# Optimization experiments

Measured on AMD Instinct MI355X. Metric: run time of the kernel, lower is better.

The kernel has to match this reference:

```python
import jax, jax.numpy as jnp
import numpy as np

NUM_NODES = 100000
EMBED_DIM = 128
COMP_DIM = 64
T = 8
NSUB = 50000


def layer_norm(x, g, b, eps=1e-5):
    mu = jnp.mean(x, axis=-1, keepdims=True)
    var = jnp.mean((x - mu) ** 2, axis=-1, keepdims=True)
    return (x - mu) * jax.lax.rsqrt(var + eps) * g + b


def setup_inputs() -> dict:
    key = jax.random.key(0)
    ks = jax.random.split(key, 12)
    D, C = EMBED_DIM, COMP_DIM
    s = lambda n: 1.0 / np.sqrt(n)
    return {
        "x": jax.random.normal(ks[0], (T * NSUB, D), dtype=jnp.float32),
        "indices": jax.random.randint(ks[1], (T, NSUB), 0, NUM_NODES, dtype=jnp.int64),
        "bd": jax.random.normal(ks[2], (NUM_NODES, D), dtype=jnp.float32),
        "ln_d_g": jnp.ones((D,), jnp.float32), "ln_d_b": jnp.zeros((D,), jnp.float32),
        "Wd1": jax.random.normal(ks[3], (D, 2 * D), jnp.float32) * s(D),
        "bd1": jnp.zeros((2 * D,), jnp.float32),
        "Wd2": jax.random.normal(ks[4], (2 * D, C), jnp.float32) * s(2 * D),
        "bd2": jnp.zeros((C,), jnp.float32),
        "ln_u_g": jnp.ones((C,), jnp.float32), "ln_u_b": jnp.zeros((C,), jnp.float32),
        "Wu1": jax.random.normal(ks[5], (C, 2 * C), jnp.float32) * s(C),
        "bu1": jnp.zeros((2 * C,), jnp.float32),
        "Wu2": jax.random.normal(ks[6], (2 * C, D), jnp.float32) * s(2 * C),
        "bu2": jnp.zeros((D,), jnp.float32),
    }


def reference(x, indices, bd, ln_d_g, ln_d_b, Wd1, bd1, Wd2, bd2,
              ln_u_g, ln_u_b, Wu1, bu1, Wu2, bu2):
    # _to_entire: per-timestep scatter-add of subnode feats into full node table
    x3 = x.reshape(T, NSUB, EMBED_DIM)  # [T, Nsub, D]
    scattered = jax.vmap(
        lambda xt, it: jax.ops.segment_sum(xt, it, num_segments=NUM_NODES)
    )(x3, indices)  # [T, num_nodes, D]
    inp = scattered + bd[None]  # ta + bd (use_bd=True)
    h = layer_norm(inp, ln_d_g, ln_d_b)
    # mlp_d: Linear -> GELU -> Dropout(eval=identity) -> Linear
    h = jax.nn.gelu(h @ Wd1 + bd1, approximate=False) @ Wd2 + bd2  # [T, num_nodes, C]
    # _from_entire: gather activated rows per timestep, then LN + mlp_u
    gathered = jax.vmap(lambda ht, it: ht[it])(h, indices)  # [T, Nsub, C]
    g = gathered.reshape(T * NSUB, COMP_DIM)
    u = layer_norm(g, ln_u_g, ln_u_b)
    out = jax.nn.gelu(u @ Wu1 + bu1, approximate=False) @ Wu2 + bu2  # [T*Nsub, D]
    return out
```

## Files before the change

### kernel.cpp

```cpp
#include <hip/hip_runtime.h>
#include <math.h>

#define NN 100000
#define DD 128
#define CC 64
#define TT 8
#define NS 50000
#define G8 8
#define MAXS2 196
#define TOTW (G8 * MAXS2)

typedef __attribute__((ext_vector_type(4))) float f32x4;
typedef __attribute__((ext_vector_type(8))) short bf16x8;
typedef unsigned short ushort_t;

__device__ __forceinline__ short f2bf(float f) {
    union { float f; unsigned u; } v; v.f = f;
    unsigned r = v.u + 0x7fffu + ((v.u >> 16) & 1u);
    return (short)(r >> 16);
}
__device__ __forceinline__ unsigned pk_bf16(float lo, float hi) {
    unsigned r;
    asm("v_cvt_pk_bf16_f32 %0, %1, %2" : "=v"(r) : "v"(lo), "v"(hi));
    return r;
}
__device__ __forceinline__ float gelu(float x) {
    float t = x + 0.044715f * x * x * x;
    return x / (1.0f + __expf(-1.5957691216f * t));
}

__global__ void prep_all(const float* __restrict__ Wd1, const float* __restrict__ Wd2,
                         const float* __restrict__ Wu1, const float* __restrict__ Wu2,
                         short* __restrict__ pW1, short* __restrict__ pW2,
                         short* __restrict__ pW3, short* __restrict__ pW4) {
    int b = blockIdx.x;
    const float* W; short* dst; int KSTEPS, total, N, s0;
    if (b < 16)      { W = Wd1; dst = pW1; KSTEPS = 4; total = 4096; N = 256; s0 = b * 256; }
    else if (b < 24) { W = Wd2; dst = pW2; KSTEPS = 8; total = 2048; N = 64;  s0 = (b - 16) * 256; }
    else if (b < 28) { W = Wu1; dst = pW3; KSTEPS = 2; total = 1024; N = 128; s0 = (b - 24) * 256; }
    else             { W = Wu2; dst = pW4; KSTEPS = 4; total = 2048; N = 128; s0 = (b - 28) * 256; }
    int s = s0 + threadIdx.x;
    if (s >= total) return;
    int lane = s & 63;
    int ks = (s >> 6) % KSTEPS;
    int n = s / (64 * KSTEPS);
    int kb = ks * 32 + (lane >> 4) * 8;
    int col = n * 16 + (lane & 15);
    bf16x8 o;
    #pragma unroll
    for (int j = 0; j < 8; ++j) o[j] = f2bf(W[(size_t)(kb + j) * N + col]);
    *(bf16x8*)(dst + (size_t)s * 8) = o;
}

__global__ void flagfill_kernel(const int* __restrict__ idx, int* __restrict__ pernode,
                                ushort_t* __restrict__ bucket) {
    int i = blockIdx.x * 256 + threadIdx.x;
    if (i >= G8 * NS) return;
    int g = i / NS, s = i - g * NS;
    int node = idx[i];
    int p = atomicAdd(&pernode[node * 8 + g], 1);
    if (p < 16) bucket[((size_t)node * 8 + g) * 16 + p] = (ushort_t)s;
}

__global__ void compact_kernel(const int* __restrict__ pernode,
                               int* __restrict__ lists, int* __restrict__ cnts) {
    int g = blockIdx.y;
    int node = blockIdx.x * 256 + threadIdx.x;
    bool active = (node < NN) && (pernode[node * 8 + g] > 0);
    unsigned long long m = __ballot(active);
    int lane = threadIdx.x & 63;
    int rank = __popcll(m & ((1ull << lane) - 1ull));
    int nact = __popcll(m);
    int lbase = 0;
    if (lane == 0 && nact > 0) lbase = atomicAdd(&cnts[g], nact);
    lbase = __shfl(lbase, 0);
    if (active) lists[(size_t)g * NS + lbase + rank] = node;
}

__global__ __launch_bounds__(1024, 4) void fused_kernel(
    const float* __restrict__ x, const float* __restrict__ bd,
    const float* __restrict__ lndg, const float* __restrict__ lndb,
    const short* __restrict__ pW1, const short* __restrict__ pW2,
    const short* __restrict__ pW3, const short* __restrict__ pW4,
    const float* __restrict__ bd1, const float* __restrict__ bd2,
    const float* __restrict__ lnug, const float* __restrict__ lnub,
    const float* __restrict__ bu1, const float* __restrict__ bu2,
    const int* __restrict__ lists, const int* __restrict__ cnts,
    const int* __restrict__ pernode, const ushort_t* __restrict__ bucket,
    float* __restrict__ out) {
    __shared__ short sW1[4096 * 8];
    __shared__ short sW2[2048 * 8];
    __shared__ short sW4[2048 * 8];
    __shared__ short sBuf[16][1024];

    const int tid = threadIdx.x;
    for (int s = tid; s < 4096; s += 1024)
        *(bf16x8*)(sW1 + s * 8) = *(const bf16x8*)(pW1 + (size_t)s * 8);
    for (int s = tid; s < 2048; s += 1024)
        *(bf16x8*)(sW2 + s * 8) = *(const bf16x8*)(pW2 + (size_t)s * 8);
    for (int s = tid; s < 2048; s += 1024)
        *(bf16x8*)(sW4 + s * 8) = *(const bf16x8*)(pW4 + (size_t)s * 8);
    __syncthreads();

    const int wave = tid >> 6, lane = tid & 63;
    short* myb = sBuf[wave];
    const int arow = lane & 15;
    const int kgrp = lane >> 4;

    int w = blockIdx.x;
    int node_c = 0, c_c = 0;
    int4 p8_c = {0, 0, 0, 0};
    {
        int g0 = w & 7, strip0 = w >> 3;
        int gi0 = strip0 * 256 + wave * 16 + arow;
        int li0 = gi0 < NS ? gi0 : NS - 1;
        node_c = lists[(size_t)g0 * NS + li0];
        c_c = pernode[node_c * 8 + g0];
        p8_c = *(const int4*)(bucket + ((size_t)node_c * 8 + g0) * 16);
    }

    for (; w < TOTW; w += gridDim.x) {
        const int g = w & 7, strip = w >> 3;
        const int nrows = cnts[g];
        const int row0 = strip * 256 + wave * 16;
        const float* x_g = x + (size_t)g * NS * DD;
        float* out_g = out + (size_t)g * NS * DD;

        const int wn = w + gridDim.x;
        const bool hn = wn < TOTW;
        const int gn = hn ? (wn & 7) : 0;
        const int stripn = hn ? (wn >> 3) : 0;
        int gin = stripn * 256 + wave * 16 + arow;
        int lin = gin < NS ? gin : NS - 1;
        const int node_n = lists[(size_t)gn * NS + lin];
        int c_n;
        int4 p8_n;

        if (strip * 256 < nrows) {
            const int c = c_c;
            const int pr0 = p8_c.x & 0xffff, pr1 = ((unsigned)p8_c.x) >> 16;
            const int pr2 = p8_c.y & 0xffff, pr3 = ((unsigned)p8_c.y) >> 16;
            float v[32];
            {
                const float* bp = bd + (size_t)node_c * DD + kgrp * 8;
                const float* xq0 = x_g + (size_t)pr0 * DD + kgrp * 8;
                const float* xq1 = x_g + (size_t)((c > 1) ? pr1 : pr0) * DD + kgrp * 8;
                const float m1 = (c > 1) ? 1.f : 0.f;
                #pragma unroll
                for (int ks = 0; ks < 4; ++ks) {
                    float4 b0 = *(const float4*)(bp + ks * 32);
                    float4 b1 = *(const float4*)(bp + ks * 32 + 4);
                    float4 a0 = *(const float4*)(xq0 + ks * 32);
                    float4 a1 = *(const float4*)(xq0 + ks * 32 + 4);
                    float4 d0 = *(const float4*)(xq1 + ks * 32);
                    float4 d1 = *(const float4*)(xq1 + ks * 32 + 4);
                    v[ks*8+0] = fmaf(m1, d0.x, b0.x + a0.x);
                    v[ks*8+1] = fmaf(m1, d0.y, b0.y + a0.y);
                    v[ks*8+2] = fmaf(m1, d0.z, b0.z + a0.z);
                    v[ks*8+3] = fmaf(m1, d0.w, b0.w + a0.w);
                    v[ks*8+4] = fmaf(m1, d1.x, b1.x + a1.x);
                    v[ks*8+5] = fmaf(m1, d1.y, b1.y + a1.y);
                    v[ks*8+6] = fmaf(m1, d1.z, b1.z + a1.z);
                    v[ks*8+7] = fmaf(m1, d1.w, b1.w + a1.w);
                }
            }
            if (__any(c > 2)) {
                const float* xq2 = x_g + (size_t)((c > 2) ? pr2 : pr0) * DD + kgrp * 8;
                const float* xq3 = x_g + (size_t)((c > 3) ? pr3 : pr0) * DD + kgrp * 8;
                const float m2 = (c > 2) ? 1.f : 0.f;
                const float m3 = (c > 3) ? 1.f : 0.f;
                #pragma unroll
                for (int ks = 0; ks < 4; ++ks) {
                    float4 a0 = *(const float4*)(xq2 + ks * 32);
                    float4 a1 = *(const float4*)(xq2 + ks * 32 + 4);
                    float4 d0 = *(const float4*)(xq3 + ks * 32);
                    float4 d1 = *(const float4*)(xq3 + ks * 32 + 4);
                    v[ks*8+0] = fmaf(m3, d0.x, fmaf(m2, a0.x, v[ks*8+0]));
                    v[ks*8+1] = fmaf(m3, d0.y, fmaf(m2, a0.y, v[ks*8+1]));
                    v[ks*8+2] = fmaf(m3, d0.z, fmaf(m2, a0.z, v[ks*8+2]));
                    v[ks*8+3] = fmaf(m3, d0.w, fmaf(m2, a0.w, v[ks*8+3]));
                    v[ks*8+4] = fmaf(m3, d1.x, fmaf(m2, a1.x, v[ks*8+4]));
                    v[ks*8+5] = fmaf(m3, d1.y, fmaf(m2, a1.y, v[ks*8+5]));
                    v[ks*8+6] = fmaf(m3, d1.z, fmaf(m2, a1.z, v[ks*8+6]));
                    v[ks*8+7] = fmaf(m3, d1.w, fmaf(m2, a1.w, v[ks*8+7]));
                }
            }
            if (__any(c > 4)) {
                const int pr4 = p8_c.z & 0xffff, pr5 = ((unsigned)p8_c.z) >> 16;
                const int pr6 = p8_c.w & 0xffff, pr7 = ((unsigned)p8_c.w) >> 16;
                const float* xq4 = x_g + (size_t)((c > 4) ? pr4 : pr0) * DD + kgrp * 8;
                const float* xq5 = x_g + (size_t)((c > 5) ? pr5 : pr0) * DD + kgrp * 8;
                const float* xq6 = x_g + (size_t)((c > 6) ? pr6 : pr0) * DD + kgrp * 8;
                const float* xq7 = x_g + (size_t)((c > 7) ? pr7 : pr0) * DD + kgrp * 8;
                const float m4 = (c > 4) ? 1.f : 0.f;
                const float m5 = (c > 5) ? 1.f : 0.f;
                const float m6 = (c > 6) ? 1.f : 0.f;
                const float m7 = (c > 7) ? 1.f : 0.f;
                #pragma unroll
                for (int ks = 0; ks < 4; ++ks) {
                    float4 a0 = *(const float4*)(xq4 + ks * 32);
                    float4 a1 = *(const float4*)(xq4 + ks * 32 + 4);
                    float4 d0 = *(const float4*)(xq5 + ks * 32);
                    float4 d1 = *(const float4*)(xq5 + ks * 32 + 4);
                    float4 e0 = *(const float4*)(xq6 + ks * 32);
                    float4 e1 = *(const float4*)(xq6 + ks * 32 + 4);
                    float4 f0 = *(const float4*)(xq7 + ks * 32);
                    float4 f1 = *(const float4*)(xq7 + ks * 32 + 4);
                    #pragma unroll
                    for (int q = 0; q < 4; ++q) {
                        float av = (&a0.x)[q], dv = (&d0.x)[q], ev = (&e0.x)[q], fv = (&f0.x)[q];
                        v[ks*8+q] = fmaf(m7, fv, fmaf(m6, ev, fmaf(m5, dv, fmaf(m4, av, v[ks*8+q]))));
                        float av1 = (&a1.x)[q], dv1 = (&d1.x)[q], ev1 = (&e1.x)[q], fv1 = (&f1.x)[q];
                        v[ks*8+4+q] = fmaf(m7, fv1, fmaf(m6, ev1, fmaf(m5, dv1, fmaf(m4, av1, v[ks*8+4+q]))));
                    }
                }
            }
            if (__any(c > 8)) {
                const ushort_t* bt = bucket + ((size_t)node_c * 8 + g) * 16;
                for (int j = 8; j < 16; ++j) {
                    const int pj = (j < c) ? bt[j] : pr0;
                    const float mj = (j < c) ? 1.f : 0.f;
                    const float* xq = x_g + (size_t)pj * DD + kgrp * 8;
                    #pragma unroll
                    for (int ks = 0; ks < 4; ++ks) {
                        float4 a0 = *(const float4*)(xq + ks * 32);
                        float4 a1 = *(const float4*)(xq + ks * 32 + 4);
                        v[ks*8+0] = fmaf(mj, a0.x, v[ks*8+0]);
                        v[ks*8+1] = fmaf(mj, a0.y, v[ks*8+1]);
                        v[ks*8+2] = fmaf(mj, a0.z, v[ks*8+2]);
                        v[ks*8+3] = fmaf(mj, a0.w, v[ks*8+3]);
                        v[ks*8+4] = fmaf(mj, a1.x, v[ks*8+4]);
                        v[ks*8+5] = fmaf(mj, a1.y, v[ks*8+5]);
                        v[ks*8+6] = fmaf(mj, a1.z, v[ks*8+6]);
                        v[ks*8+7] = fmaf(mj, a1.w, v[ks*8+7]);
                    }
                }
            }
            float s1 = 0.f;
            #pragma unroll
            for (int j = 0; j < 32; ++j) s1 += v[j];
            s1 += __shfl_xor(s1, 16); s1 += __shfl_xor(s1, 32);
            float mu = s1 * 0.0078125f;
            float s2 = 0.f;
            #pragma unroll
            for (int j = 0; j < 32; ++j) { float d = v[j] - mu; s2 += d * d; }
            s2 += __shfl_xor(s2, 16); s2 += __shfl_xor(s2, 32);
            float rs = rsqrtf(s2 * 0.0078125f + 1e-5f);
            union U8 { bf16x8 v8; unsigned u[4]; };
            bf16x8 afr[4];
            {
                const float* gp = lndg + kgrp * 8;
                const float* bbp = lndb + kgrp * 8;
                #pragma unroll
                for (int ks = 0; ks < 4; ++ks) {
                    float4 g0 = *(const float4*)(gp + ks * 32);
                    float4 g1 = *(const float4*)(gp + ks * 32 + 4);
                    float4 c0 = *(const float4*)(bbp + ks * 32);
                    float4 c1 = *(const float4*)(bbp + ks * 32 + 4);
                    U8 t;
                    t.u[0] = pk_bf16((v[ks*8+0]-mu)*rs*g0.x + c0.x, (v[ks*8+1]-mu)*rs*g0.y + c0.y);
                    t.u[1] = pk_bf16((v[ks*8+2]-mu)*rs*g0.z + c0.z, (v[ks*8+3]-mu)*rs*g0.w + c0.w);
                    t.u[2] = pk_bf16((v[ks*8+4]-mu)*rs*g1.x + c1.x, (v[ks*8+5]-mu)*rs*g1.y + c1.y);
                    t.u[3] = pk_bf16((v[ks*8+6]-mu)*rs*g1.z + c1.z, (v[ks*8+7]-mu)*rs*g1.w + c1.w);
                    afr[ks] = t.v8;
                }
            }
            f32x4 acc2[4];
            #pragma unroll
            for (int n = 0; n < 4; ++n) acc2[n] = (f32x4){0.f, 0.f, 0.f, 0.f};
            for (int ks2 = 0; ks2 < 8; ++ks2) {
                f32x4 a1v[2];
                a1v[0] = (f32x4){0.f, 0.f, 0.f, 0.f};
                a1v[1] = (f32x4){0.f, 0.f, 0.f, 0.f};
                #pragma unroll
                for (int ks1 = 0; ks1 < 4; ++ks1) {
                    #pragma unroll
                    for (int p = 0; p < 2; ++p) {
                        bf16x8 bf = *(const bf16x8*)(sW1 + (size_t)((((2*ks2+p) << 2) | ks1) * 64 + lane) * 8);
                        a1v[p] = __builtin_amdgcn_mfma_f32_16x16x32_bf16(afr[ks1], bf, a1v[p], 0, 0, 0);
                    }
                }
                #pragma unroll
                for (int p = 0; p < 2; ++p) {
                    float bias = bd1[(2*ks2+p) * 16 + arow];
                    #pragma unroll
                    for (int rr = 0; rr < 4; ++rr) {
                        float vv = gelu(a1v[p][rr] + bias);
                        int row = kgrp * 4 + rr;
                        int byte = row * 64 + (((p * 16 + arow) * 2) ^ ((row & 3) << 4));
                        myb[byte >> 1] = f2bf(vv);
                    }
                }
                bf16x8 af2 = *(const bf16x8*)(myb + ((arow * 64 + ((kgrp * 16) ^ ((arow & 3) << 4))) >> 1));
                #pragma unroll
                for (int n2 = 0; n2 < 4; ++n2) {
                    bf16x8 bf = *(const bf16x8*)(sW2 + (size_t)(((n2 << 3) | ks2) * 64 + lane) * 8);
                    acc2[n2] = __builtin_amdgcn_mfma_f32_16x16x32_bf16(af2, bf, acc2[n2], 0, 0, 0);
                }
            }
            c_n = pernode[node_n * 8 + gn];
            p8_n = *(const int4*)(bucket + ((size_t)node_n * 8 + gn) * 16);
            float hv[4][4];
            #pragma unroll
            for (int n2 = 0; n2 < 4; ++n2)
                #pragma unroll
                for (int rr = 0; rr < 4; ++rr)
                    hv[n2][rr] = acc2[n2][rr] + bd2[n2 * 16 + arow];
            float mu_u[4], rs_u[4];
            #pragma unroll
            for (int rr = 0; rr < 4; ++rr) {
                float sr = hv[0][rr] + hv[1][rr] + hv[2][rr] + hv[3][rr];
                sr += __shfl_xor(sr, 1); sr += __shfl_xor(sr, 2);
                sr += __shfl_xor(sr, 4); sr += __shfl_xor(sr, 8);
                mu_u[rr] = sr * 0.015625f;
                float sq = 0.f;
                #pragma unroll
                for (int n2 = 0; n2 < 4; ++n2) { float d = hv[n2][rr] - mu_u[rr]; sq += d * d; }
                sq += __shfl_xor(sq, 1); sq += __shfl_xor(sq, 2);
                sq += __shfl_xor(sq, 4); sq += __shfl_xor(sq, 8);
                rs_u[rr] = rsqrtf(sq * 0.015625f + 1e-5f);
            }
            #pragma unroll
            for (int n2 = 0; n2 < 4; ++n2) {
                int cidx = n2 * 16 + arow;
                float gg = lnug[cidx], bb = lnub[cidx];
                #pragma unroll
                for (int rr = 0; rr < 4; ++rr) {
                    float nv = (hv[n2][rr] - mu_u[rr]) * rs_u[rr] * gg + bb;
                    int row = kgrp * 4 + rr;
                    int byte = row * 128 + ((cidx * 2) ^ ((row & 7) << 4));
                    myb[byte >> 1] = f2bf(nv);
                }
            }
            bf16x8 af3[2];
            #pragma unroll
            for (int ks3 = 0; ks3 < 2; ++ks3)
                af3[ks3] = *(const bf16x8*)(myb + ((arow * 128 + ((ks3 * 64 + kgrp * 16) ^ ((arow & 7) << 4))) >> 1));
            f32x4 acc4[8];
            #pragma unroll
            for (int n = 0; n < 8; ++n) acc4[n] = (f32x4){0.f, 0.f, 0.f, 0.f};
            #pragma unroll
            for (int half = 0; half < 2; ++half) {
                f32x4 a3[4];
                #pragma unroll
                for (int n = 0; n < 4; ++n) a3[n] = (f32x4){0.f, 0.f, 0.f, 0.f};
                #pragma unroll
                for (int ks3 = 0; ks3 < 2; ++ks3) {
                    #pragma unroll
                    for (int n3h = 0; n3h < 4; ++n3h) {
                        int n3 = half * 4 + n3h;
                        bf16x8 bf = *(const bf16x8*)(pW3 + (size_t)(((n3 << 1) | ks3) * 64 + lane) * 8);
                        a3[n3h] = __builtin_amdgcn_mfma_f32_16x16x32_bf16(af3[ks3], bf, a3[n3h], 0, 0, 0);
                    }
                }
                #pragma unroll
                for (int n3h = 0; n3h < 4; ++n3h) {
                    float bias = bu1[(half * 4 + n3h) * 16 + arow];
                    #pragma unroll
                    for (int rr = 0; rr < 4; ++rr) {
                        float vv = gelu(a3[n3h][rr] + bias);
                        int row = kgrp * 4 + rr;
                        int byte = row * 128 + (((n3h * 16 + arow) * 2) ^ ((row & 7) << 4));
                        myb[byte >> 1] = f2bf(vv);
                    }
                }
                #pragma unroll
                for (int k4 = 0; k4 < 2; ++k4) {
                    bf16x8 afu = *(const bf16x8*)(myb + ((arow * 128 + ((k4 * 64 + kgrp * 16) ^ ((arow & 7) << 4))) >> 1));
                    #pragma unroll
                    for (int n4 = 0; n4 < 8; ++n4) {
                        bf16x8 bf = *(const bf16x8*)(sW4 + (size_t)(((n4 << 2) | (half * 2 + k4)) * 64 + lane) * 8);
                        acc4[n4] = __builtin_amdgcn_mfma_f32_16x16x32_bf16(afu, bf, acc4[n4], 0, 0, 0);
                    }
                }
            }
            #pragma unroll
            for (int rr = 0; rr < 4; ++rr) {
                const int src = kgrp * 4 + rr;
                const int c2  = __shfl(c_c, src);
                const unsigned w0 = (unsigned)__shfl(p8_c.x, src);
                const unsigned w1 = (unsigned)__shfl(p8_c.y, src);
                const unsigned w2 = (unsigned)__shfl(p8_c.z, src);
                const unsigned w3 = (unsigned)__shfl(p8_c.w, src);
                const int nd  = __shfl(node_c, src);
                const int gi2 = row0 + kgrp * 4 + rr;
                if (gi2 >= nrows) continue;
                float vals[8];
                #pragma unroll
                for (int n4 = 0; n4 < 8; ++n4) vals[n4] = acc4[n4][rr] + bu2[n4 * 16 + arow];
                {
                    float* op = out_g + (size_t)(w0 & 0xffff) * DD + arow;
                    #pragma unroll
                    for (int n4 = 0; n4 < 8; ++n4) op[n4 * 16] = vals[n4];
                }
                if (c2 > 1) {
                    float* op = out_g + (size_t)(w0 >> 16) * DD + arow;
                    #pragma unroll
                    for (int n4 = 0; n4 < 8; ++n4) op[n4 * 16] = vals[n4];
                }
                if (c2 > 2) {
                    float* op = out_g + (size_t)(w1 & 0xffff) * DD + arow;
                    #pragma unroll
                    for (int n4 = 0; n4 < 8; ++n4) op[n4 * 16] = vals[n4];
                }
                if (c2 > 3) {
                    float* op = out_g + (size_t)(w1 >> 16) * DD + arow;
                    #pragma unroll
                    for (int n4 = 0; n4 < 8; ++n4) op[n4 * 16] = vals[n4];
                }
                if (__any(c2 > 4)) {
                    if (c2 > 4) {
                        float* op = out_g + (size_t)(w2 & 0xffff) * DD + arow;
                        #pragma unroll
                        for (int n4 = 0; n4 < 8; ++n4) op[n4 * 16] = vals[n4];
                    }
                    if (c2 > 5) {
                        float* op = out_g + (size_t)(w2 >> 16) * DD + arow;
                        #pragma unroll
                        for (int n4 = 0; n4 < 8; ++n4) op[n4 * 16] = vals[n4];
                    }
                    if (c2 > 6) {
                        float* op = out_g + (size_t)(w3 & 0xffff) * DD + arow;
                        #pragma unroll
                        for (int n4 = 0; n4 < 8; ++n4) op[n4 * 16] = vals[n4];
                    }
                    if (c2 > 7) {
                        float* op = out_g + (size_t)(w3 >> 16) * DD + arow;
                        #pragma unroll
                        for (int n4 = 0; n4 < 8; ++n4) op[n4 * 16] = vals[n4];
                    }
                }
                if (__any(c2 > 8)) {
                    const ushort_t* bt = bucket + ((size_t)nd * 8 + g) * 16;
                    for (int j = 8; j < 16; ++j) {
                        if (j < c2) {
                            float* op = out_g + (size_t)bt[j] * DD + arow;
                            #pragma unroll
                            for (int n4 = 0; n4 < 8; ++n4) op[n4 * 16] = vals[n4];
                        }
                    }
                }
            }
        } else {
            c_n = pernode[node_n * 8 + gn];
            p8_n = *(const int4*)(bucket + ((size_t)node_n * 8 + gn) * 16);
        }
        node_c = node_n; c_c = c_n; p8_c = p8_n;
    }
}

extern "C" void kernel_launch(void* const* d_in, const int* in_sizes, int n_in,
                              void* d_out, int out_size, void* d_ws, size_t ws_size,
                              hipStream_t stream) {
    const float* x       = (const float*)d_in[0];
    const int*   indices = (const int*)d_in[1];
    const float* bd      = (const float*)d_in[2];
    const float* ln_d_g  = (const float*)d_in[3];
    const float* ln_d_b  = (const float*)d_in[4];
    const float* Wd1     = (const float*)d_in[5];
    const float* bd1     = (const float*)d_in[6];
    const float* Wd2     = (const float*)d_in[7];
    const float* bd2     = (const float*)d_in[8];
    const float* ln_u_g  = (const float*)d_in[9];
    const float* ln_u_b  = (const float*)d_in[10];
    const float* Wu1     = (const float*)d_in[11];
    const float* bu1     = (const float*)d_in[12];
    const float* Wu2     = (const float*)d_in[13];
    const float* bu2     = (const float*)d_in[14];
    float* out = (float*)d_out;

    char* ws = (char*)d_ws;
    size_t o = 0;
    auto alloc_b = [&](size_t bytes) { char* p = ws + o; o = (o + bytes + 255) & ~(size_t)255; return p; };
    int*      pernode = (int*)alloc_b((size_t)NN * 8 * 4);
    int*      cnts    = (int*)alloc_b(8 * 4);
    int*      lists   = (int*)alloc_b((size_t)8 * NS * 4);
    size_t zero_bytes = (size_t)((char*)lists - (char*)pernode) + (size_t)8 * NS * 4;
    ushort_t* bucket  = (ushort_t*)alloc_b((size_t)NN * 8 * 16 * 2);
    short*    pW1     = (short*)alloc_b((size_t)4096 * 16);
    short*    pW2     = (short*)alloc_b((size_t)2048 * 16);
    short*    pW3     = (short*)alloc_b((size_t)1024 * 16);
    short*    pW4     = (short*)alloc_b((size_t)2048 * 16);

    hipMemsetAsync(pernode, 0, zero_bytes, stream);

    prep_all<<<36, 256, 0, stream>>>(Wd1, Wd2, Wu1, Wu2, pW1, pW2, pW3, pW4);
    flagfill_kernel<<<(G8 * NS + 255) / 256, 256, 0, stream>>>(indices, pernode, bucket);
    compact_kernel<<<dim3((NN + 255) / 256, G8), 256, 0, stream>>>(pernode, lists, cnts);
    fused_kernel<<<256, 1024, 0, stream>>>(x, bd, ln_d_g, ln_d_b, pW1, pW2, pW3, pW4,
                                           bd1, bd2, ln_u_g, ln_u_b, bu1, bu2,
                                           lists, cnts, pernode, bucket, out);
}
```

Before: 483.0 us.

## Split work into singleton-node and multi-hit-node paths with separate lists

Nodes hit exactly once per timestep are listed by subnode index and handled on a lean path: one x row plus bd, one output store, no bucket lookup and no masked multi-row accumulation. Nodes hit two or more times go to a second list and keep the bucket-based accumulation and multi-store path. The shared LN/MLP code is factored into device helpers, and the software prefetch of the next tile's node metadata is removed. The aim is to cut wasted loads and divergence on the common singleton case. The cost is two tile ranges to schedule, no cross-iteration prefetch, and a fixed cap of 25000 entries per timestep on the multi-hit list.

```diff
diff --git a/kernel.cpp b/kernel.cpp
--- a/kernel.cpp
+++ b/kernel.cpp
@@ -7,8 +7,9 @@
 #define TT 8
 #define NS 50000
 #define G8 8
-#define MAXS2 196
-#define TOTW (G8 * MAXS2)
+#define T1MAX (G8 * 196)
+#define T2MAX (G8 * 98)
+#define L2CAP 25000
 
 typedef __attribute__((ext_vector_type(4))) float f32x4;
 typedef __attribute__((ext_vector_type(8))) short bf16x8;
@@ -62,30 +63,185 @@
     if (p < 16) bucket[((size_t)node * 8 + g) * 16 + p] = (ushort_t)s;
 }
 
-__global__ void compact_kernel(const int* __restrict__ pernode,
-                               int* __restrict__ lists, int* __restrict__ cnts) {
+__global__ void compact2_kernel(const int* __restrict__ idx, const int* __restrict__ pernode,
+                                int* __restrict__ list1, int* __restrict__ cnts1,
+                                int* __restrict__ list2, int* __restrict__ cnts2) {
     int g = blockIdx.y;
-    int node = blockIdx.x * 256 + threadIdx.x;
-    bool active = (node < NN) && (pernode[node * 8 + g] > 0);
-    unsigned long long m = __ballot(active);
+    int i = blockIdx.x * 256 + threadIdx.x;
     int lane = threadIdx.x & 63;
-    int rank = __popcll(m & ((1ull << lane) - 1ull));
-    int nact = __popcll(m);
-    int lbase = 0;
-    if (lane == 0 && nact > 0) lbase = atomicAdd(&cnts[g], nact);
-    lbase = __shfl(lbase, 0);
-    if (active) lists[(size_t)g * NS + lbase + rank] = node;
+    bool a1 = false;
+    if (i < NS) {
+        int nd = idx[(size_t)g * NS + i];
+        a1 = (pernode[nd * 8 + g] == 1);
+    }
+    unsigned long long m1 = __ballot(a1);
+    int r1 = __popcll(m1 & ((1ull << lane) - 1ull));
+    int c1 = __popcll(m1);
+    int b1 = 0;
+    if (lane == 0 && c1 > 0) b1 = atomicAdd(&cnts1[g], c1);
+    b1 = __shfl(b1, 0);
+    if (a1) list1[(size_t)g * NS + b1 + r1] = i;
+    bool a2 = (i < NN) && (pernode[i * 8 + g] >= 2);
+    unsigned long long m2 = __ballot(a2);
+    int r2 = __popcll(m2 & ((1ull << lane) - 1ull));
+    int c2 = __popcll(m2);
+    int b2 = 0;
+    if (lane == 0 && c2 > 0) b2 = atomicAdd(&cnts2[g], c2);
+    b2 = __shfl(b2, 0);
+    if (a2) list2[(size_t)g * L2CAP + b2 + r2] = i;
+}
+
+__device__ __forceinline__ void mlp_core(
+    const bf16x8 (&afr)[4], short* myb, int arow, int kgrp,
+    const short* sW1, const short* sW2, const short* __restrict__ pW3, const short* sW4,
+    const float* __restrict__ bd1, const float* __restrict__ bd2,
+    const float* __restrict__ lnug, const float* __restrict__ lnub,
+    const float* __restrict__ bu1, f32x4 (&acc4)[8]) {
+    f32x4 acc2[4];
+    #pragma unroll
+    for (int n = 0; n < 4; ++n) acc2[n] = (f32x4){0.f, 0.f, 0.f, 0.f};
+    for (int ks2 = 0; ks2 < 8; ++ks2) {
+        f32x4 a1v[2];
+        a1v[0] = (f32x4){0.f, 0.f, 0.f, 0.f};
+        a1v[1] = (f32x4){0.f, 0.f, 0.f, 0.f};
+        #pragma unroll
+        for (int ks1 = 0; ks1 < 4; ++ks1) {
+            #pragma unroll
+            for (int p = 0; p < 2; ++p) {
+                bf16x8 bf = *(const bf16x8*)(sW1 + (size_t)((((2 * ks2 + p) << 2) | ks1) * 64 + (kgrp * 16 + arow)) * 8);
+                a1v[p] = __builtin_amdgcn_mfma_f32_16x16x32_bf16(afr[ks1], bf, a1v[p], 0, 0, 0);
+            }
+        }
+        #pragma unroll
+        for (int p = 0; p < 2; ++p) {
+            float bias = bd1[(2 * ks2 + p) * 16 + arow];
+            #pragma unroll
+            for (int rr = 0; rr < 4; ++rr) {
+                float vv = gelu(a1v[p][rr] + bias);
+                int row = kgrp * 4 + rr;
+                int byte = row * 64 + (((p * 16 + arow) * 2) ^ ((row & 3) << 4));
+                myb[byte >> 1] = f2bf(vv);
+            }
+        }
+        bf16x8 af2 = *(const bf16x8*)(myb + ((arow * 64 + ((kgrp * 16) ^ ((arow & 3) << 4))) >> 1));
+        #pragma unroll
+        for (int n2 = 0; n2 < 4; ++n2) {
+            bf16x8 bf = *(const bf16x8*)(sW2 + (size_t)(((n2 << 3) | ks2) * 64 + (kgrp * 16 + arow)) * 8);
+            acc2[n2] = __builtin_amdgcn_mfma_f32_16x16x32_bf16(af2, bf, acc2[n2], 0, 0, 0);
+        }
+    }
+    float hv[4][4];
+    #pragma unroll
+    for (int n2 = 0; n2 < 4; ++n2)
+        #pragma unroll
+        for (int rr = 0; rr < 4; ++rr)
+            hv[n2][rr] = acc2[n2][rr] + bd2[n2 * 16 + arow];
+    #pragma unroll
+    for (int rr = 0; rr < 4; ++rr) {
+        float sr = hv[0][rr] + hv[1][rr] + hv[2][rr] + hv[3][rr];
+        sr += __shfl_xor(sr, 1); sr += __shfl_xor(sr, 2);
+        sr += __shfl_xor(sr, 4); sr += __shfl_xor(sr, 8);
+        float mu_u = sr * 0.015625f;
+        float sq = 0.f;
+        #pragma unroll
+        for (int n2 = 0; n2 < 4; ++n2) { float d = hv[n2][rr] - mu_u; sq += d * d; }
+        sq += __shfl_xor(sq, 1); sq += __shfl_xor(sq, 2);
+        sq += __shfl_xor(sq, 4); sq += __shfl_xor(sq, 8);
+        float rs_u = rsqrtf(sq * 0.015625f + 1e-5f);
+        #pragma unroll
+        for (int n2 = 0; n2 < 4; ++n2) {
+            int cidx = n2 * 16 + arow;
+            float nv = (hv[n2][rr] - mu_u) * rs_u * lnug[cidx] + lnub[cidx];
+            int row = kgrp * 4 + rr;
+            int byte = row * 128 + ((cidx * 2) ^ ((row & 7) << 4));
+            myb[byte >> 1] = f2bf(nv);
+        }
+    }
+    bf16x8 af3[2];
+    #pragma unroll
+    for (int ks3 = 0; ks3 < 2; ++ks3)
+        af3[ks3] = *(const bf16x8*)(myb + ((arow * 128 + ((ks3 * 64 + kgrp * 16) ^ ((arow & 7) << 4))) >> 1));
+    #pragma unroll
+    for (int n = 0; n < 8; ++n) acc4[n] = (f32x4){0.f, 0.f, 0.f, 0.f};
+    #pragma unroll
+    for (int half = 0; half < 2; ++half) {
+        f32x4 a3[4];
+        #pragma unroll
+        for (int n = 0; n < 4; ++n) a3[n] = (f32x4){0.f, 0.f, 0.f, 0.f};
+        #pragma unroll
+        for (int ks3 = 0; ks3 < 2; ++ks3) {
+            #pragma unroll
+            for (int n3h = 0; n3h < 4; ++n3h) {
+                int n3 = half * 4 + n3h;
+                bf16x8 bf = *(const bf16x8*)(pW3 + (size_t)(((n3 << 1) | ks3) * 64 + (kgrp * 16 + arow)) * 8);
+                a3[n3h] = __builtin_amdgcn_mfma_f32_16x16x32_bf16(af3[ks3], bf, a3[n3h], 0, 0, 0);
+            }
+        }
+        #pragma unroll
+        for (int n3h = 0; n3h < 4; ++n3h) {
+            float bias = bu1[(half * 4 + n3h) * 16 + arow];
+            #pragma unroll
+            for (int rr = 0; rr < 4; ++rr) {
+                float vv = gelu(a3[n3h][rr] + bias);
+                int row = kgrp * 4 + rr;
+                int byte = row * 128 + (((n3h * 16 + arow) * 2) ^ ((row & 7) << 4));
+                myb[byte >> 1] = f2bf(vv);
+            }
+        }
+        #pragma unroll
+        for (int k4 = 0; k4 < 2; ++k4) {
+            bf16x8 afu = *(const bf16x8*)(myb + ((arow * 128 + ((k4 * 64 + kgrp * 16) ^ ((arow & 7) << 4))) >> 1));
+            #pragma unroll
+            for (int n4 = 0; n4 < 8; ++n4) {
+                bf16x8 bf = *(const bf16x8*)(sW4 + (size_t)(((n4 << 2) | (half * 2 + k4)) * 64 + (kgrp * 16 + arow)) * 8);
+                acc4[n4] = __builtin_amdgcn_mfma_f32_16x16x32_bf16(afu, bf, acc4[n4], 0, 0, 0);
+            }
+        }
+    }
+}
+
+__device__ __forceinline__ void ln_d_pack(
+    const float (&v)[32], int kgrp,
+    const float* __restrict__ lndg, const float* __restrict__ lndb, bf16x8 (&afr)[4]) {
+    float s1 = 0.f;
+    #pragma unroll
+    for (int j = 0; j < 32; ++j) s1 += v[j];
+    s1 += __shfl_xor(s1, 16); s1 += __shfl_xor(s1, 32);
+    float mu = s1 * 0.0078125f;
+    float s2 = 0.f;
+    #pragma unroll
+    for (int j = 0; j < 32; ++j) { float d = v[j] - mu; s2 += d * d; }
+    s2 += __shfl_xor(s2, 16); s2 += __shfl_xor(s2, 32);
+    float rs = rsqrtf(s2 * 0.0078125f + 1e-5f);
+    union U8 { bf16x8 v8; unsigned u[4]; };
+    const float* gp = lndg + kgrp * 8;
+    const float* bbp = lndb + kgrp * 8;
+    #pragma unroll
+    for (int ks = 0; ks < 4; ++ks) {
+        float4 g0 = *(const float4*)(gp + ks * 32);
+        float4 g1 = *(const float4*)(gp + ks * 32 + 4);
+        float4 c0 = *(const float4*)(bbp + ks * 32);
+        float4 c1 = *(const float4*)(bbp + ks * 32 + 4);
+        U8 t;
+        t.u[0] = pk_bf16((v[ks*8+0]-mu)*rs*g0.x + c0.x, (v[ks*8+1]-mu)*rs*g0.y + c0.y);
+        t.u[1] = pk_bf16((v[ks*8+2]-mu)*rs*g0.z + c0.z, (v[ks*8+3]-mu)*rs*g0.w + c0.w);
+        t.u[2] = pk_bf16((v[ks*8+4]-mu)*rs*g1.x + c1.x, (v[ks*8+5]-mu)*rs*g1.y + c1.y);
+        t.u[3] = pk_bf16((v[ks*8+6]-mu)*rs*g1.z + c1.z, (v[ks*8+7]-mu)*rs*g1.w + c1.w);
+        afr[ks] = t.v8;
+    }
 }
 
 __global__ __launch_bounds__(1024, 4) void fused_kernel(
-    const float* __restrict__ x, const float* __restrict__ bd,
+    const float* __restrict__ x, const int* __restrict__ idx,
+    const float* __restrict__ bd,
     const float* __restrict__ lndg, const float* __restrict__ lndb,
     const short* __restrict__ pW1, const short* __restrict__ pW2,
     const short* __restrict__ pW3, const short* __restrict__ pW4,
     const float* __restrict__ bd1, const float* __restrict__ bd2,
     const float* __restrict__ lnug, const float* __restrict__ lnub,
     const float* __restrict__ bu1, const float* __restrict__ bu2,
-    const int* __restrict__ lists, const int* __restrict__ cnts,
+    const int* __restrict__ list1, const int* __restrict__ cnts1,
+    const int* __restrict__ list2, const int* __restrict__ cnts2,
     const int* __restrict__ pernode, const ushort_t* __restrict__ bucket,
     float* __restrict__ out) {
     __shared__ short sW1[4096 * 8];
@@ -107,45 +263,66 @@
     const int arow = lane & 15;
     const int kgrp = lane >> 4;
 
-    int w = blockIdx.x;
-    int node_c = 0, c_c = 0;
-    int4 p8_c = {0, 0, 0, 0};
-    {
-        int g0 = w & 7, strip0 = w >> 3;
-        int gi0 = strip0 * 256 + wave * 16 + arow;
-        int li0 = gi0 < NS ? gi0 : NS - 1;
-        node_c = lists[(size_t)g0 * NS + li0];
-        c_c = pernode[node_c * 8 + g0];
-        p8_c = *(const int4*)(bucket + ((size_t)node_c * 8 + g0) * 16);
-    }
-
-    for (; w < TOTW; w += gridDim.x) {
-        const int g = w & 7, strip = w >> 3;
-        const int nrows = cnts[g];
-        const int row0 = strip * 256 + wave * 16;
-        const float* x_g = x + (size_t)g * NS * DD;
-        float* out_g = out + (size_t)g * NS * DD;
-
-        const int wn = w + gridDim.x;
-        const bool hn = wn < TOTW;
-        const int gn = hn ? (wn & 7) : 0;
-        const int stripn = hn ? (wn >> 3) : 0;
-        int gin = stripn * 256 + wave * 16 + arow;
-        int lin = gin < NS ? gin : NS - 1;
-        const int node_n = lists[(size_t)gn * NS + lin];
-        int c_n;
-        int4 p8_n;
-
-        if (strip * 256 < nrows) {
-            const int c = c_c;
-            const int pr0 = p8_c.x & 0xffff, pr1 = ((unsigned)p8_c.x) >> 16;
-            const int pr2 = p8_c.y & 0xffff, pr3 = ((unsigned)p8_c.y) >> 16;
+    for (int w = blockIdx.x; w < T1MAX + T2MAX; w += gridDim.x) {
+        if (w < T1MAX) {
+            const int g = w & 7, strip = w >> 3;
+            const int n1g = cnts1[g];
+            const int row0 = strip * 256 + wave * 16;
+            if (row0 >= n1g) continue;
+            const float* x_g = x + (size_t)g * NS * DD;
+            float* out_g = out + (size_t)g * NS * DD;
+            const int gi = row0 + arow;
+            const int s_val = list1[(size_t)g * NS + (gi < n1g ? gi : n1g - 1)];
+            const int node = idx[(size_t)g * NS + s_val];
             float v[32];
             {
-                const float* bp = bd + (size_t)node_c * DD + kgrp * 8;
+                const float* xp = x_g + (size_t)s_val * DD + kgrp * 8;
+                const float* bp = bd + (size_t)node * DD + kgrp * 8;
+                #pragma unroll
+                for (int ks = 0; ks < 4; ++ks) {
+                    float4 a0 = *(const float4*)(xp + ks * 32);
+                    float4 a1 = *(const float4*)(xp + ks * 32 + 4);
+                    float4 b0 = *(const float4*)(bp + ks * 32);
+                    float4 b1 = *(const float4*)(bp + ks * 32 + 4);
+                    v[ks*8+0] = a0.x + b0.x; v[ks*8+1] = a0.y + b0.y;
+                    v[ks*8+2] = a0.z + b0.z; v[ks*8+3] = a0.w + b0.w;
+                    v[ks*8+4] = a1.x + b1.x; v[ks*8+5] = a1.y + b1.y;
+                    v[ks*8+6] = a1.z + b1.z; v[ks*8+7] = a1.w + b1.w;
+                }
+            }
+            bf16x8 afr[4];
+            ln_d_pack(v, kgrp, lndg, lndb, afr);
+            f32x4 acc4[8];
+            mlp_core(afr, myb, arow, kgrp, sW1, sW2, pW3, sW4,
+                     bd1, bd2, lnug, lnub, bu1, acc4);
+            #pragma unroll
+            for (int rr = 0; rr < 4; ++rr) {
+                const int src = kgrp * 4 + rr;
+                const int s2v = __shfl(s_val, src);
+                if (row0 + src >= n1g) continue;
+                float* op = out_g + (size_t)s2v * DD + arow;
+                #pragma unroll
+                for (int n4 = 0; n4 < 8; ++n4)
+                    op[n4 * 16] = acc4[n4][rr] + bu2[n4 * 16 + arow];
+            }
+        } else {
+            const int w2 = w - T1MAX;
+            const int g = w2 & 7, strip = w2 >> 3;
+            const int n2g = cnts2[g];
+            const int row0 = strip * 256 + wave * 16;
+            if (row0 >= n2g) continue;
+            const float* x_g = x + (size_t)g * NS * DD;
+            float* out_g = out + (size_t)g * NS * DD;
+            const int gi = row0 + arow;
+            const int node = list2[(size_t)g * L2CAP + (gi < n2g ? gi : n2g - 1)];
+            const int c = pernode[node * 8 + g];
+            const int4 p8 = *(const int4*)(bucket + ((size_t)node * 8 + g) * 16);
+            const int pr0 = p8.x & 0xffff, pr1 = ((unsigned)p8.x) >> 16;
+            float v[32];
+            {
+                const float* bp = bd + (size_t)node * DD + kgrp * 8;
                 const float* xq0 = x_g + (size_t)pr0 * DD + kgrp * 8;
-                const float* xq1 = x_g + (size_t)((c > 1) ? pr1 : pr0) * DD + kgrp * 8;
-                const float m1 = (c > 1) ? 1.f : 0.f;
+                const float* xq1 = x_g + (size_t)pr1 * DD + kgrp * 8;
                 #pragma unroll
                 for (int ks = 0; ks < 4; ++ks) {
                     float4 b0 = *(const float4*)(bp + ks * 32);
@@ -154,17 +331,18 @@
                     float4 a1 = *(const float4*)(xq0 + ks * 32 + 4);
                     float4 d0 = *(const float4*)(xq1 + ks * 32);
                     float4 d1 = *(const float4*)(xq1 + ks * 32 + 4);
-                    v[ks*8+0] = fmaf(m1, d0.x, b0.x + a0.x);
-                    v[ks*8+1] = fmaf(m1, d0.y, b0.y + a0.y);
-                    v[ks*8+2] = fmaf(m1, d0.z, b0.z + a0.z);
-                    v[ks*8+3] = fmaf(m1, d0.w, b0.w + a0.w);
-                    v[ks*8+4] = fmaf(m1, d1.x, b1.x + a1.x);
-                    v[ks*8+5] = fmaf(m1, d1.y, b1.y + a1.y);
-                    v[ks*8+6] = fmaf(m1, d1.z, b1.z + a1.z);
-                    v[ks*8+7] = fmaf(m1, d1.w, b1.w + a1.w);
+                    v[ks*8+0] = b0.x + a0.x + d0.x;
+                    v[ks*8+1] = b0.y + a0.y + d0.y;
+                    v[ks*8+2] = b0.z + a0.z + d0.z;
+                    v[ks*8+3] = b0.w + a0.w + d0.w;
+                    v[ks*8+4] = b1.x + a1.x + d1.x;
+                    v[ks*8+5] = b1.y + a1.y + d1.y;
+                    v[ks*8+6] = b1.z + a1.z + d1.z;
+                    v[ks*8+7] = b1.w + a1.w + d1.w;
                 }
             }
             if (__any(c > 2)) {
+                const int pr2 = p8.y & 0xffff, pr3 = ((unsigned)p8.y) >> 16;
                 const float* xq2 = x_g + (size_t)((c > 2) ? pr2 : pr0) * DD + kgrp * 8;
                 const float* xq3 = x_g + (size_t)((c > 3) ? pr3 : pr0) * DD + kgrp * 8;
                 const float m2 = (c > 2) ? 1.f : 0.f;
@@ -186,266 +364,77 @@
                 }
             }
             if (__any(c > 4)) {
-                const int pr4 = p8_c.z & 0xffff, pr5 = ((unsigned)p8_c.z) >> 16;
-                const int pr6 = p8_c.w & 0xffff, pr7 = ((unsigned)p8_c.w) >> 16;
-                const float* xq4 = x_g + (size_t)((c > 4) ? pr4 : pr0) * DD + kgrp * 8;
-                const float* xq5 = x_g + (size_t)((c > 5) ? pr5 : pr0) * DD + kgrp * 8;
-                const float* xq6 = x_g + (size_t)((c > 6) ? pr6 : pr0) * DD + kgrp * 8;
-                const float* xq7 = x_g + (size_t)((c > 7) ? pr7 : pr0) * DD + kgrp * 8;
-                const float m4 = (c > 4) ? 1.f : 0.f;
-                const float m5 = (c > 5) ? 1.f : 0.f;
-                const float m6 = (c > 6) ? 1.f : 0.f;
-                const float m7 = (c > 7) ? 1.f : 0.f;
-                #pragma unroll
-                for (int ks = 0; ks < 4; ++ks) {
-                    float4 a0 = *(const float4*)(xq4 + ks * 32);
-                    float4 a1 = *(const float4*)(xq4 + ks * 32 + 4);
-                    float4 d0 = *(const float4*)(xq5 + ks * 32);
-                    float4 d1 = *(const float4*)(xq5 + ks * 32 + 4);
-                    float4 e0 = *(const float4*)(xq6 + ks * 32);
-                    float4 e1 = *(const float4*)(xq6 + ks * 32 + 4);
-                    float4 f0 = *(const float4*)(xq7 + ks * 32);
-                    float4 f1 = *(const float4*)(xq7 + ks * 32 + 4);
-                    #pragma unroll
-                    for (int q = 0; q < 4; ++q) {
-                        float av = (&a0.x)[q], dv = (&d0.x)[q], ev = (&e0.x)[q], fv = (&f0.x)[q];
-                        v[ks*8+q] = fmaf(m7, fv, fmaf(m6, ev, fmaf(m5, dv, fmaf(m4, av, v[ks*8+q]))));
-                        float av1 = (&a1.x)[q], dv1 = (&d1.x)[q], ev1 = (&e1.x)[q], fv1 = (&f1.x)[q];
-                        v[ks*8+4+q] = fmaf(m7, fv1, fmaf(m6, ev1, fmaf(m5, dv1, fmaf(m4, av1, v[ks*8+4+q]))));
-                    }
-                }
-            }
-            if (__any(c > 8)) {
-                const ushort_t* bt = bucket + ((size_t)node_c * 8 + g) * 16;
-                for (int j = 8; j < 16; ++j) {
-                    const int pj = (j < c) ? bt[j] : pr0;
-                    const float mj = (j < c) ? 1.f : 0.f;
-                    const float* xq = x_g + (size_t)pj * DD + kgrp * 8;
+                const ushort_t* bt = bucket + ((size_t)node * 8 + g) * 16;
+                for (int j = 4; j < 16; j += 2) {
+                    if (!__any(c > j)) break;
+                    const int pa = (j < c) ? bt[j] : pr0;
+                    const int pb = (j + 1 < c) ? bt[j + 1] : pr0;
+                    const float ma = (j < c) ? 1.f : 0.f;
+                    const float mb = (j + 1 < c) ? 1.f : 0.f;
+                    const float* xqa = x_g + (size_t)pa * DD + kgrp * 8;
+                    const float* xqb = x_g + (size_t)pb * DD + kgrp * 8;
                     #pragma unroll
                     for (int ks = 0; ks < 4; ++ks) {
-                        float4 a0 = *(const float4*)(xq + ks * 32);
-                        float4 a1 = *(const float4*)(xq + ks * 32 + 4);
-                        v[ks*8+0] = fmaf(mj, a0.x, v[ks*8+0]);
-                        v[ks*8+1] = fmaf(mj, a0.y, v[ks*8+1]);
-                        v[ks*8+2] = fmaf(mj, a0.z, v[ks*8+2]);
-                        v[ks*8+3] = fmaf(mj, a0.w, v[ks*8+3]);
-                        v[ks*8+4] = fmaf(mj, a1.x, v[ks*8+4]);
-                        v[ks*8+5] = fmaf(mj, a1.y, v[ks*8+5]);
-                        v[ks*8+6] = fmaf(mj, a1.z, v[ks*8+6]);
-                        v[ks*8+7] = fmaf(mj, a1.w, v[ks*8+7]);
+                        float4 a0 = *(const float4*)(xqa + ks * 32);
+                        float4 a1 = *(const float4*)(xqa + ks * 32 + 4);
+                        float4 d0 = *(const float4*)(xqb + ks * 32);
+                        float4 d1 = *(const float4*)(xqb + ks * 32 + 4);
+                        v[ks*8+0] = fmaf(mb, d0.x, fmaf(ma, a0.x, v[ks*8+0]));
+                        v[ks*8+1] = fmaf(mb, d0.y, fmaf(ma, a0.y, v[ks*8+1]));
+                        v[ks*8+2] = fmaf(mb, d0.z, fmaf(ma, a0.z, v[ks*8+2]));
+                        v[ks*8+3] = fmaf(mb, d0.w, fmaf(ma, a0.w, v[ks*8+3]));
+                        v[ks*8+4] = fmaf(mb, d1.x, fmaf(ma, a1.x, v[ks*8+4]));
+                        v[ks*8+5] = fmaf(mb, d1.y, fmaf(ma, a1.y, v[ks*8+5]));
+                        v[ks*8+6] = fmaf(mb, d1.z, fmaf(ma, a1.z, v[ks*8+6]));
+                        v[ks*8+7] = fmaf(mb, d1.w, fmaf(ma, a1.w, v[ks*8+7]));
                     }
                 }
             }
-            float s1 = 0.f;
-            #pragma unroll
-            for (int j = 0; j < 32; ++j) s1 += v[j];
-            s1 += __shfl_xor(s1, 16); s1 += __shfl_xor(s1, 32);
-            float mu = s1 * 0.0078125f;
-            float s2 = 0.f;
-            #pragma unroll
-            for (int j = 0; j < 32; ++j) { float d = v[j] - mu; s2 += d * d; }
-            s2 += __shfl_xor(s2, 16); s2 += __shfl_xor(s2, 32);
-            float rs = rsqrtf(s2 * 0.0078125f + 1e-5f);
-            union U8 { bf16x8 v8; unsigned u[4]; };
             bf16x8 afr[4];
-            {
-                const float* gp = lndg + kgrp * 8;
-                const float* bbp = lndb + kgrp * 8;
-                #pragma unroll
-                for (int ks = 0; ks < 4; ++ks) {
-                    float4 g0 = *(const float4*)(gp + ks * 32);
-                    float4 g1 = *(const float4*)(gp + ks * 32 + 4);
-                    float4 c0 = *(const float4*)(bbp + ks * 32);
-                    float4 c1 = *(const float4*)(bbp + ks * 32 + 4);
-                    U8 t;
-                    t.u[0] = pk_bf16((v[ks*8+0]-mu)*rs*g0.x + c0.x, (v[ks*8+1]-mu)*rs*g0.y + c0.y);
-                    t.u[1] = pk_bf16((v[ks*8+2]-mu)*rs*g0.z + c0.z, (v[ks*8+3]-mu)*rs*g0.w + c0.w);
-                    t.u[2] = pk_bf16((v[ks*8+4]-mu)*rs*g1.x + c1.x, (v[ks*8+5]-mu)*rs*g1.y + c1.y);
-                    t.u[3] = pk_bf16((v[ks*8+6]-mu)*rs*g1.z + c1.z, (v[ks*8+7]-mu)*rs*g1.w + c1.w);
-                    afr[ks] = t.v8;
-                }
-            }
-            f32x4 acc2[4];
-            #pragma unroll
-            for (int n = 0; n < 4; ++n) acc2[n] = (f32x4){0.f, 0.f, 0.f, 0.f};
-            for (int ks2 = 0; ks2 < 8; ++ks2) {
-                f32x4 a1v[2];
-                a1v[0] = (f32x4){0.f, 0.f, 0.f, 0.f};
-                a1v[1] = (f32x4){0.f, 0.f, 0.f, 0.f};
-                #pragma unroll
-                for (int ks1 = 0; ks1 < 4; ++ks1) {
-                    #pragma unroll
-                    for (int p = 0; p < 2; ++p) {
-                        bf16x8 bf = *(const bf16x8*)(sW1 + (size_t)((((2*ks2+p) << 2) | ks1) * 64 + lane) * 8);
-                        a1v[p] = __builtin_amdgcn_mfma_f32_16x16x32_bf16(afr[ks1], bf, a1v[p], 0, 0, 0);
-                    }
-                }
-                #pragma unroll
-                for (int p = 0; p < 2; ++p) {
-                    float bias = bd1[(2*ks2+p) * 16 + arow];
-                    #pragma unroll
-                    for (int rr = 0; rr < 4; ++rr) {
-                        float vv = gelu(a1v[p][rr] + bias);
-                        int row = kgrp * 4 + rr;
-                        int byte = row * 64 + (((p * 16 + arow) * 2) ^ ((row & 3) << 4));
-                        myb[byte >> 1] = f2bf(vv);
-                    }
-                }
-                bf16x8 af2 = *(const bf16x8*)(myb + ((arow * 64 + ((kgrp * 16) ^ ((arow & 3) << 4))) >> 1));
-                #pragma unroll
-                for (int n2 = 0; n2 < 4; ++n2) {
-                    bf16x8 bf = *(const bf16x8*)(sW2 + (size_t)(((n2 << 3) | ks2) * 64 + lane) * 8);
-                    acc2[n2] = __builtin_amdgcn_mfma_f32_16x16x32_bf16(af2, bf, acc2[n2], 0, 0, 0);
-                }
-            }
-            c_n = pernode[node_n * 8 + gn];
-            p8_n = *(const int4*)(bucket + ((size_t)node_n * 8 + gn) * 16);
-            float hv[4][4];
-            #pragma unroll
-            for (int n2 = 0; n2 < 4; ++n2)
-                #pragma unroll
-                for (int rr = 0; rr < 4; ++rr)
-                    hv[n2][rr] = acc2[n2][rr] + bd2[n2 * 16 + arow];
-            float mu_u[4], rs_u[4];
+            ln_d_pack(v, kgrp, lndg, lndb, afr);
+            f32x4 acc4[8];
+            mlp_core(afr, myb, arow, kgrp, sW1, sW2, pW3, sW4,
+                     bd1, bd2, lnug, lnub, bu1, acc4);
             #pragma unroll
             for (int rr = 0; rr < 4; ++rr) {
-                float sr = hv[0][rr] + hv[1][rr] + hv[2][rr] + hv[3][rr];
-                sr += __shfl_xor(sr, 1); sr += __shfl_xor(sr, 2);
-                sr += __shfl_xor(sr, 4); sr += __shfl_xor(sr, 8);
-                mu_u[rr] = sr * 0.015625f;
-                float sq = 0.f;
-                #pragma unroll
-                for (int n2 = 0; n2 < 4; ++n2) { float d = hv[n2][rr] - mu_u[rr]; sq += d * d; }
-                sq += __shfl_xor(sq, 1); sq += __shfl_xor(sq, 2);
-                sq += __shfl_xor(sq, 4); sq += __shfl_xor(sq, 8);
-                rs_u[rr] = rsqrtf(sq * 0.015625f + 1e-5f);
-            }
-            #pragma unroll
-            for (int n2 = 0; n2 < 4; ++n2) {
-                int cidx = n2 * 16 + arow;
-                float gg = lnug[cidx], bb = lnub[cidx];
-                #pragma unroll
-                for (int rr = 0; rr < 4; ++rr) {
-                    float nv = (hv[n2][rr] - mu_u[rr]) * rs_u[rr] * gg + bb;
-                    int row = kgrp * 4 + rr;
-                    int byte = row * 128 + ((cidx * 2) ^ ((row & 7) << 4));
-                    myb[byte >> 1] = f2bf(nv);
-                }
-            }
-            bf16x8 af3[2];
-            #pragma unroll
-            for (int ks3 = 0; ks3 < 2; ++ks3)
-                af3[ks3] = *(const bf16x8*)(myb + ((arow * 128 + ((ks3 * 64 + kgrp * 16) ^ ((arow & 7) << 4))) >> 1));
-            f32x4 acc4[8];
-            #pragma unroll
-            for (int n = 0; n < 8; ++n) acc4[n] = (f32x4){0.f, 0.f, 0.f, 0.f};
-            #pragma unroll
-            for (int half = 0; half < 2; ++half) {
-                f32x4 a3[4];
-                #pragma unroll
-                for (int n = 0; n < 4; ++n) a3[n] = (f32x4){0.f, 0.f, 0.f, 0.f};
-                #pragma unroll
-                for (int ks3 = 0; ks3 < 2; ++ks3) {
-                    #pragma unroll
-                    for (int n3h = 0; n3h < 4; ++n3h) {
-                        int n3 = half * 4 + n3h;
-                        bf16x8 bf = *(const bf16x8*)(pW3 + (size_t)(((n3 << 1) | ks3) * 64 + lane) * 8);
-                        a3[n3h] = __builtin_amdgcn_mfma_f32_16x16x32_bf16(af3[ks3], bf, a3[n3h], 0, 0, 0);
-                    }
-                }
-                #pragma unroll
-                for (int n3h = 0; n3h < 4; ++n3h) {
-                    float bias = bu1[(half * 4 + n3h) * 16 + arow];
-                    #pragma unroll
-                    for (int rr = 0; rr < 4; ++rr) {
-                        float vv = gelu(a3[n3h][rr] + bias);
-                        int row = kgrp * 4 + rr;
-                        int byte = row * 128 + (((n3h * 16 + arow) * 2) ^ ((row & 7) << 4));
-                        myb[byte >> 1] = f2bf(vv);
-                    }
-                }
-                #pragma unroll
-                for (int k4 = 0; k4 < 2; ++k4) {
-                    bf16x8 afu = *(const bf16x8*)(myb + ((arow * 128 + ((k4 * 64 + kgrp * 16) ^ ((arow & 7) << 4))) >> 1));
-                    #pragma unroll
-                    for (int n4 = 0; n4 < 8; ++n4) {
-                        bf16x8 bf = *(const bf16x8*)(sW4 + (size_t)(((n4 << 2) | (half * 2 + k4)) * 64 + lane) * 8);
-                        acc4[n4] = __builtin_amdgcn_mfma_f32_16x16x32_bf16(afu, bf, acc4[n4], 0, 0, 0);
-                    }
-                }
-            }
-            #pragma unroll
-            for (int rr = 0; rr < 4; ++rr) {
-                const int src = kgrp * 4 + rr;
-                const int c2  = __shfl(c_c, src);
-                const unsigned w0 = (unsigned)__shfl(p8_c.x, src);
-                const unsigned w1 = (unsigned)__shfl(p8_c.y, src);
-                const unsigned w2 = (unsigned)__shfl(p8_c.z, src);
-                const unsigned w3 = (unsigned)__shfl(p8_c.w, src);
-                const int nd  = __shfl(node_c, src);
                 const int gi2 = row0 + kgrp * 4 + rr;
-                if (gi2 >= nrows) continue;
+                if (gi2 >= n2g) continue;
+                const int nd = list2[(size_t)g * L2CAP + gi2];
+                const int c2 = pernode[nd * 8 + g];
+                const ushort_t* bt = bucket + ((size_t)nd * 8 + g) * 16;
+                const int4 q4 = *(const int4*)bt;
                 float vals[8];
                 #pragma unroll
                 for (int n4 = 0; n4 < 8; ++n4) vals[n4] = acc4[n4][rr] + bu2[n4 * 16 + arow];
                 {
-                    float* op = out_g + (size_t)(w0 & 0xffff) * DD + arow;
+                    float* op = out_g + (size_t)(q4.x & 0xffff) * DD + arow;
                     #pragma unroll
                     for (int n4 = 0; n4 < 8; ++n4) op[n4 * 16] = vals[n4];
                 }
-                if (c2 > 1) {
-                    float* op = out_g + (size_t)(w0 >> 16) * DD + arow;
+                {
+                    float* op = out_g + (size_t)(((unsigned)q4.x) >> 16) * DD + arow;
                     #pragma unroll
                     for (int n4 = 0; n4 < 8; ++n4) op[n4 * 16] = vals[n4];
                 }
                 if (c2 > 2) {
-                    float* op = out_g + (size_t)(w1 & 0xffff) * DD + arow;
+                    float* op = out_g + (size_t)(q4.y & 0xffff) * DD + arow;
                     #pragma unroll
                     for (int n4 = 0; n4 < 8; ++n4) op[n4 * 16] = vals[n4];
                 }
                 if (c2 > 3) {
-                    float* op = out_g + (size_t)(w1 >> 16) * DD + arow;
+                    float* op = out_g + (size_t)(((unsigned)q4.y) >> 16) * DD + arow;
                     #pragma unroll
                     for (int n4 = 0; n4 < 8; ++n4) op[n4 * 16] = vals[n4];
                 }
-                if (__any(c2 > 4)) {
-                    if (c2 > 4) {
-                        float* op = out_g + (size_t)(w2 & 0xffff) * DD + arow;
+                if (c2 > 4) {
+                    for (int j = 4; j < c2 && j < 16; ++j) {
+                        float* op = out_g + (size_t)bt[j] * DD + arow;
                         #pragma unroll
                         for (int n4 = 0; n4 < 8; ++n4) op[n4 * 16] = vals[n4];
                     }
-                    if (c2 > 5) {
-                        float* op = out_g + (size_t)(w2 >> 16) * DD + arow;
-                        #pragma unroll
-                        for (int n4 = 0; n4 < 8; ++n4) op[n4 * 16] = vals[n4];
-                    }
-                    if (c2 > 6) {
-                        float* op = out_g + (size_t)(w3 & 0xffff) * DD + arow;
-                        #pragma unroll
-                        for (int n4 = 0; n4 < 8; ++n4) op[n4 * 16] = vals[n4];
-                    }
-                    if (c2 > 7) {
-                        float* op = out_g + (size_t)(w3 >> 16) * DD + arow;
-                        #pragma unroll
-                        for (int n4 = 0; n4 < 8; ++n4) op[n4 * 16] = vals[n4];
-                    }
-                }
-                if (__any(c2 > 8)) {
-                    const ushort_t* bt = bucket + ((size_t)nd * 8 + g) * 16;
-                    for (int j = 8; j < 16; ++j) {
-                        if (j < c2) {
-                            float* op = out_g + (size_t)bt[j] * DD + arow;
-                            #pragma unroll
-                            for (int n4 = 0; n4 < 8; ++n4) op[n4 * 16] = vals[n4];
-                        }
-                    }
-                }
-            }
-        } else {
-            c_n = pernode[node_n * 8 + gn];
-            p8_n = *(const int4*)(bucket + ((size_t)node_n * 8 + gn) * 16);
-        }
-        node_c = node_n; c_c = c_n; p8_c = p8_n;
+                }
+            }
+        }
     }
 }
 
@@ -473,9 +462,11 @@
     size_t o = 0;
     auto alloc_b = [&](size_t bytes) { char* p = ws + o; o = (o + bytes + 255) & ~(size_t)255; return p; };
     int*      pernode = (int*)alloc_b((size_t)NN * 8 * 4);
-    int*      cnts    = (int*)alloc_b(8 * 4);
-    int*      lists   = (int*)alloc_b((size_t)8 * NS * 4);
-    size_t zero_bytes = (size_t)((char*)lists - (char*)pernode) + (size_t)8 * NS * 4;
+    int*      cnts1   = (int*)alloc_b(8 * 4);
+    int*      cnts2   = (int*)alloc_b(8 * 4);
+    size_t zero_bytes = (size_t)((char*)cnts2 - (char*)pernode) + 256;
+    int*      list1   = (int*)alloc_b((size_t)8 * NS * 4);
+    int*      list2   = (int*)alloc_b((size_t)8 * L2CAP * 4);
     ushort_t* bucket  = (ushort_t*)alloc_b((size_t)NN * 8 * 16 * 2);
     short*    pW1     = (short*)alloc_b((size_t)4096 * 16);
     short*    pW2     = (short*)alloc_b((size_t)2048 * 16);
@@ -486,8 +477,12 @@
 
     prep_all<<<36, 256, 0, stream>>>(Wd1, Wd2, Wu1, Wu2, pW1, pW2, pW3, pW4);
     flagfill_kernel<<<(G8 * NS + 255) / 256, 256, 0, stream>>>(indices, pernode, bucket);
-    compact_kernel<<<dim3((NN + 255) / 256, G8), 256, 0, stream>>>(pernode, lists, cnts);
-    fused_kernel<<<256, 1024, 0, stream>>>(x, bd, ln_d_g, ln_d_b, pW1, pW2, pW3, pW4,
+    compact2_kernel<<<dim3((NN + 255) / 256, G8), 256, 0, stream>>>(indices, pernode,
+                                                                    list1, cnts1,
+                                                                    list2, cnts2);
+    fused_kernel<<<256, 1024, 0, stream>>>(x, indices, bd, ln_d_g, ln_d_b,
+                                           pW1, pW2, pW3, pW4,
                                            bd1, bd2, ln_u_g, ln_u_b, bu1, bu2,
-                                           lists, cnts, pernode, bucket, out);
-}
+                                           list1, cnts1, list2, cnts2,
+                                           pernode, bucket, out);
+}
```

New measurement: 495.1 us. 1.03x slower.
